# Kernel tuning notes

Measured on AMD Instinct MI355X. Metric: run time of the kernel, lower is better.

## Reference

```python
import jax, jax.numpy as jnp
import numpy as np

N_HEAD, DIM, D_K, D_V = 16, 1024, 64, 64
B, L = 4, 2048


def setup_inputs() -> dict:
    key = jax.random.key(0)
    ks = jax.random.split(key, 8)
    def xavier(k, shape, fan_in, fan_out):
        std = float(np.sqrt(2.0 / (fan_in + fan_out)))
        return jax.random.normal(k, shape, dtype=jnp.float32) * std
    return {
        "q": jax.random.normal(ks[0], (B, L, DIM), dtype=jnp.float32),
        "k": jax.random.normal(ks[1], (B, L, DIM), dtype=jnp.float32),
        "v": jax.random.normal(ks[2], (B, L, DIM), dtype=jnp.float32),
        "w_q": xavier(ks[3], (N_HEAD, DIM, D_K), DIM, D_K),
        "w_k": xavier(ks[4], (N_HEAD, DIM, D_K), DIM, D_K),
        "w_v": xavier(ks[5], (N_HEAD, DIM, D_V), DIM, D_V),
        "proj_w": xavier(ks[6], (DIM, N_HEAD * D_V), N_HEAD * D_V, DIM),
        "proj_b": jnp.zeros((DIM,), dtype=jnp.float32),
    }


def reference(q, k, v, w_q, w_k, w_v, proj_w, proj_b):
    batch, len_q, dim = q.shape
    # NOTE: original scales by sqrt(dim) (model dim), not sqrt(d_k)
    scale = jnp.asarray(np.sqrt(dim), dtype=q.dtype)
    # per-head projections: [h, b, q, dk]
    qh = jnp.einsum('bqd,hdk->hbqk', q, w_q)
    kh = jnp.einsum('bsd,hdk->hbsk', k, w_k)
    vh = jnp.einsum('bsd,hdv->hbsv', v, w_v)
    scores = jnp.einsum('hbqk,hbsk->hbqs', qh, kh) / scale
    attn = jax.nn.softmax(scores, axis=-1)
    out = jnp.einsum('hbqs,hbsv->hbqv', attn, vh)
    # concat heads along last dim: [b, q, h*dv] (head-major order, matching torch.cat(split))
    out = jnp.transpose(out, (1, 2, 0, 3)).reshape(batch, len_q, -1)
    # output projection (dropout is identity at eval)
    return out @ proj_w.T + proj_b
```

## Files before the change

kernel.cpp:

```cpp
#include <hip/hip_runtime.h>
#include <hip/hip_bf16.h>
#include <stdint.h>

#define NH 16
#define DM 1024
#define DKV 64
#define BB 4
#define LL 2048
#define MT (BB*LL)
#define NT (LL/64)

typedef __bf16 bf16;
typedef __bf16 bf16x8 __attribute__((ext_vector_type(8)));
typedef float f32x4 __attribute__((ext_vector_type(4)));
typedef float f32x16 __attribute__((ext_vector_type(16)));
typedef unsigned int u32x2 __attribute__((ext_vector_type(2)));
typedef unsigned int u32x4 __attribute__((ext_vector_type(4)));

__device__ __forceinline__ void gload_lds16(const void* g, void* l) {
  __builtin_amdgcn_global_load_lds(
      (const __attribute__((address_space(1))) unsigned int*)g,
      (__attribute__((address_space(3))) unsigned int*)l, 16, 0, 0);
}

__device__ __forceinline__ unsigned short bfbits(float x) {
  bf16 b = (bf16)x;
  return __builtin_bit_cast(unsigned short, b);
}

__device__ __forceinline__ float fast_exp2(float x) {
#if defined(__has_builtin)
#if __has_builtin(__builtin_amdgcn_exp2f)
  return __builtin_amdgcn_exp2f(x);
#else
  float r; asm("v_exp_f32 %0, %1" : "=v"(r) : "v"(x)); return r;
#endif
#else
  float r; asm("v_exp_f32 %0, %1" : "=v"(r) : "v"(x)); return r;
#endif
}

#if defined(__has_builtin)
#if __has_builtin(__builtin_amdgcn_permlane32_swap)
#define HAVE_PLSWAP 1
#endif
#endif

__device__ __forceinline__ u32x2 plswap(unsigned int a, unsigned int b, int hi) {
#ifdef HAVE_PLSWAP
  auto rr = __builtin_amdgcn_permlane32_swap(a, b, false, false);
  u32x2 r; r.x = rr[0]; r.y = rr[1];
  return r;
#else
  unsigned int pa = (unsigned int)__shfl_xor((int)a, 32);
  unsigned int pb_ = (unsigned int)__shfl_xor((int)b, 32);
  u32x2 r;
  r.x = hi ? pb_ : a;
  r.y = hi ? b : pa;
  return r;
#endif
}

__device__ __forceinline__ bf16x8 pack8(const f32x4& lo, const f32x4& hi2) {
  u32x4 u;
  u.x = (unsigned int)bfbits(lo[0]) | ((unsigned int)bfbits(lo[1]) << 16);
  u.y = (unsigned int)bfbits(lo[2]) | ((unsigned int)bfbits(lo[3]) << 16);
  u.z = (unsigned int)bfbits(hi2[0]) | ((unsigned int)bfbits(hi2[1]) << 16);
  u.w = (unsigned int)bfbits(hi2[2]) | ((unsigned int)bfbits(hi2[3]) << 16);
  return __builtin_bit_cast(bf16x8, u);
}

__global__ __launch_bounds__(256) void prep_w(const float* __restrict__ w0, const float* __restrict__ w1,
                                              const float* __restrict__ w2, const float* __restrict__ pw,
                                              bf16* __restrict__ o0, bf16* __restrict__ o1,
                                              bf16* __restrict__ o2, bf16* __restrict__ Wp) {
  __shared__ float t[64][65];
  if (blockIdx.z < 3) {
    const float* w = blockIdx.z == 0 ? w0 : (blockIdx.z == 1 ? w1 : w2);
    bf16* o = blockIdx.z == 0 ? o0 : (blockIdx.z == 1 ? o1 : o2);
    int h = blockIdx.y, d0 = blockIdx.x * 64;
    const float* src = w + ((size_t)h * DM + d0) * DKV;
    for (int i = threadIdx.x; i < 64 * 64; i += 256) {
      int r = i >> 6, c = i & 63;
      t[r][c] = src[(size_t)r * DKV + c];
    }
    __syncthreads();
    for (int i = threadIdx.x; i < 64 * 64; i += 256) {
      int kk = i >> 6, d = i & 63;
      o[((size_t)(h * 64 + kk)) * DM + d0 + d] = (bf16)t[d][kk];
    }
  } else {
    int base = ((blockIdx.y * 16 + blockIdx.x) * 256 + threadIdx.x) * 2;
#pragma unroll
    for (int e = 0; e < 2; ++e) {
      int i = base + e;
      const float4* p = (const float4*)pw + (size_t)i * 2;
      float4 a = p[0], b = p[1];
      bf16x8 r;
      r[0] = (bf16)a.x; r[1] = (bf16)a.y; r[2] = (bf16)a.z; r[3] = (bf16)a.w;
      r[4] = (bf16)b.x; r[5] = (bf16)b.y; r[6] = (bf16)b.z; r[7] = (bf16)b.w;
      *((bf16x8*)Wp + i) = r;
    }
  }
}

__global__ __launch_bounds__(256, 3) void gemm_qkv(const float* __restrict__ Qf, const float* __restrict__ Kf,
                                                   const float* __restrict__ Vf, const bf16* __restrict__ Wqt,
                                                   const bf16* __restrict__ Wkt, const bf16* __restrict__ Wvt,
                                                   bf16* __restrict__ QH, bf16* __restrict__ KH,
                                                   bf16* __restrict__ VT) {
  __shared__ bf16 sA[128 * 64];
  __shared__ bf16 sB[128 * 64];
  const int bid = blockIdx.x;
  const int xcd = bid & 7;
  const int j   = bid >> 3;
  const int nb  = j & 7;
  const int t   = j >> 3;
  const int mb  = xcd + 8 * (t & 7);
  const int mode = t >> 3;
  const float* A = mode == 0 ? Qf : (mode == 1 ? Kf : Vf);
  const bf16* Bt = mode == 0 ? Wqt : (mode == 1 ? Wkt : Wvt);
  const int tid = threadIdx.x;
  const int w = tid >> 6, l = tid & 63;
  const int c = l & 15, g4 = l >> 4;
  const int wm = w >> 1, wn = w & 1;
  const int m0 = mb * 128, n0 = nb * 128;

  int grow[4], gsg[4];
#pragma unroll
  for (int jj = 0; jj < 4; ++jj) {
    int gi = jj * 256 + tid;
    grow[jj] = gi >> 3;
    gsg[jj] = (gi & 7) ^ (grow[jj] & 7);
  }

  f32x4 ra[4][2];
  u32x4 rbr[4];

  auto LOADA = [&](int kt) {
#pragma unroll
    for (int jj = 0; jj < 4; ++jj) {
      const float* s = A + (size_t)(m0 + grow[jj]) * 1024 + kt + gsg[jj] * 8;
      ra[jj][0] = *(const f32x4*)s;
      ra[jj][1] = *(const f32x4*)(s + 4);
    }
  };
  auto LOADB = [&](int kt) {
#pragma unroll
    for (int jj = 0; jj < 4; ++jj)
      rbr[jj] = *(const u32x4*)(Bt + (size_t)(n0 + grow[jj]) * 1024 + kt + gsg[jj] * 8);
  };
  auto WRITE = [&]() {
#pragma unroll
    for (int jj = 0; jj < 4; ++jj) {
      *(bf16x8*)((char*)sA + (jj * 256 + tid) * 16) = pack8(ra[jj][0], ra[jj][1]);
      *(u32x4*)((char*)sB + (jj * 256 + tid) * 16) = rbr[jj];
    }
  };

  f32x4 acc[4][4] = {};
  LOADA(0); LOADB(0);
  for (int it = 0; it < 16; ++it) {
    WRITE();
    if (it < 15) { LOADA((it + 1) * 64); LOADB((it + 1) * 64); }
    asm volatile("s_waitcnt lgkmcnt(0)" ::: "memory");
    __builtin_amdgcn_s_barrier();
#pragma unroll
    for (int ks = 0; ks < 2; ++ks) {
      bf16x8 af[4], bfr[4];
#pragma unroll
      for (int x = 0; x < 4; ++x) {
        int ar = wm * 64 + x * 16 + c;
        af[x] = *(const bf16x8*)((const char*)sA + ar * 128 + (((ks * 4 + g4) ^ (ar & 7)) * 16));
        int br = wn * 64 + x * 16 + c;
        bfr[x] = *(const bf16x8*)((const char*)sB + br * 128 + (((ks * 4 + g4) ^ (br & 7)) * 16));
      }
      __builtin_amdgcn_s_setprio(1);
#pragma unroll
      for (int x = 0; x < 4; ++x)
#pragma unroll
        for (int y = 0; y < 4; ++y)
          acc[x][y] = __builtin_amdgcn_mfma_f32_16x16x32_bf16(af[x], bfr[y], acc[x][y], 0, 0, 0);
      __builtin_amdgcn_s_setprio(0);
    }
    __builtin_amdgcn_s_barrier();
  }

  const int mm = m0 + wm * 64, nn = n0 + wn * 64;
  if (mode < 2) {
    bf16* O = mode == 0 ? QH : KH;
    const float s = (mode == 0) ? 0.03125f * 1.44269504088896f : 1.0f;
#pragma unroll
    for (int x = 0; x < 4; ++x)
#pragma unroll
      for (int y = 0; y < 4; ++y)
#pragma unroll
        for (int r = 0; r < 4; ++r) {
          int m = mm + x * 16 + g4 * 4 + r;
          int n = nn + y * 16 + c;
          O[(size_t)m * 1024 + n] = (bf16)(acc[x][y][r] * s);
        }
  } else {
    bf16* O = VT;
#pragma unroll
    for (int x = 0; x < 4; ++x)
#pragma unroll
      for (int y = 0; y < 4; ++y) {
        int mb2 = mm + x * 16 + g4 * 4;
        int n = nn + y * 16 + c;
        int bb2 = mb2 >> 11, sidx = mb2 & 2047;
        int hh2 = n >> 6, dv = n & 63;
        unsigned int u0 = bfbits(acc[x][y][0]) | ((unsigned int)bfbits(acc[x][y][1]) << 16);
        unsigned int u1 = bfbits(acc[x][y][2]) | ((unsigned int)bfbits(acc[x][y][3]) << 16);
        *(uint2*)(O + ((size_t)((hh2 * 4 + bb2) * 64 + dv)) * LL + sidx) = make_uint2(u0, u1);
      }
  }
}

__global__ __launch_bounds__(256) void gemm_proj(const bf16* __restrict__ A, const bf16* __restrict__ Bt,
                                                 float* __restrict__ Out, const float* __restrict__ bias) {
  __shared__ bf16 sA[128 * 64];
  __shared__ bf16 sB[128 * 64];
  const int bid = blockIdx.x;
  const int xcd = bid & 7;
  const int j = bid >> 3;
  const int nb = j & 7;
  const int mb = xcd + 8 * (j >> 3);
  const int tid = threadIdx.x;
  const int w = tid >> 6, l = tid & 63;
  const int c = l & 15, g4 = l >> 4;
  const int wm = w >> 1, wn = w & 1;
  const int m0 = mb * 128, n0 = nb * 128;

  f32x4 acc[4][4] = {};
  for (int kt = 0; kt < 1024; kt += 64) {
#pragma unroll
    for (int i = 0; i < 4; ++i) {
      int blk = i * 4 + w;
      int row = blk * 8 + (l >> 3);
      int g = (l & 7) ^ (row & 7);
      gload_lds16(A + ((size_t)(m0 + row)) * 1024 + kt + g * 8, (char*)sA + blk * 1024);
      gload_lds16(Bt + ((size_t)(n0 + row)) * 1024 + kt + g * 8, (char*)sB + blk * 1024);
    }
    __syncthreads();
#pragma unroll
    for (int ks = 0; ks < 2; ++ks) {
      bf16x8 af[4], bfr[4];
#pragma unroll
      for (int x = 0; x < 4; ++x) {
        int ar = wm * 64 + x * 16 + c;
        af[x] = *(const bf16x8*)((const char*)sA + ar * 128 + (((ks * 4 + g4) ^ (ar & 7)) * 16));
        int br = wn * 64 + x * 16 + c;
        bfr[x] = *(const bf16x8*)((const char*)sB + br * 128 + (((ks * 4 + g4) ^ (br & 7)) * 16));
      }
#pragma unroll
      for (int x = 0; x < 4; ++x)
#pragma unroll
        for (int y = 0; y < 4; ++y)
          acc[x][y] = __builtin_amdgcn_mfma_f32_16x16x32_bf16(af[x], bfr[y], acc[x][y], 0, 0, 0);
    }
    __syncthreads();
  }

  const int mm = m0 + wm * 64, nn = n0 + wn * 64;
#pragma unroll
  for (int x = 0; x < 4; ++x)
#pragma unroll
    for (int y = 0; y < 4; ++y)
#pragma unroll
      for (int r = 0; r < 4; ++r) {
        int m = mm + x * 16 + g4 * 4 + r;
        int n = nn + y * 16 + c;
        Out[(size_t)m * 1024 + n] = acc[x][y][r] + bias[n];
      }
}

__global__ __launch_bounds__(256, 2) void attn_kernel(const bf16* __restrict__ qh,
                                                      const bf16* __restrict__ kh,
                                                      const bf16* __restrict__ vt,
                                                      bf16* __restrict__ o) {
  __shared__ bf16 sK[4][64 * 64];
  __shared__ bf16 sV[4][64 * 64];
  const int tid = threadIdx.x, w = tid >> 6, l = tid & 63;
  const int c = l & 31, hi = l >> 5;
  const int bh = blockIdx.x, b = bh & 3, h = bh >> 2;
  const int q0 = blockIdx.y * 256 + w * 64;

  const bf16* qbase = qh + ((size_t)(b * LL)) * DM + h * 64;
  const bf16* kbase = kh + ((size_t)(b * LL)) * DM + h * 64;
  const bf16* vbase = vt + ((size_t)((h * 4 + b) * 64)) * LL;

  bf16x8 qfA[4], qfB[4];
#pragma unroll
  for (int ks = 0; ks < 4; ++ks) {
    qfA[ks] = *(const bf16x8*)(qbase + (size_t)(q0 + c) * DM + ks * 16 + hi * 8);
    qfB[ks] = *(const bf16x8*)(qbase + (size_t)(q0 + 32 + c) * DM + ks * 16 + hi * 8);
  }

  bf16x8 onesf;
#pragma unroll
  for (int i = 0; i < 8; ++i) onesf[i] = (bf16)1.0f;

  f32x16 oA0 = {}, oA1 = {}, oB0 = {}, oB1 = {};
  f32x16 lAa = {}, lBa = {};

  auto STAGE = [&](int bufi, int kv0) {
#pragma unroll
    for (int j = 0; j < 2; ++j) {
      int gi = w * 128 + j * 64 + l;
      int row = gi >> 3;
      int g = (gi & 7) ^ (row & 7);
      gload_lds16(kbase + (size_t)(kv0 + row) * DM + g * 8,
                  (char*)sK[bufi] + (w * 128 + j * 64) * 16);
      gload_lds16(vbase + (size_t)row * LL + kv0 + g * 8,
                  (char*)sV[bufi] + (w * 128 + j * 64) * 16);
    }
  };

  auto EXPPACK = [&](f32x16& st0, f32x16& st1, bf16x8* pb) {
#pragma unroll
    for (int r = 0; r < 16; ++r) st0[r] = fast_exp2(st0[r]);
#pragma unroll
    for (int r = 0; r < 16; ++r) st1[r] = fast_exp2(st1[r]);
#pragma unroll
    for (int t = 0; t < 2; ++t) {
      const f32x16& st = t ? st1 : st0;
      unsigned int u[4][2];
#pragma unroll
      for (int g2 = 0; g2 < 4; ++g2) {
        u[g2][0] = (unsigned int)bfbits(st[4 * g2 + 0]) | ((unsigned int)bfbits(st[4 * g2 + 1]) << 16);
        u[g2][1] = (unsigned int)bfbits(st[4 * g2 + 2]) | ((unsigned int)bfbits(st[4 * g2 + 3]) << 16);
      }
      u32x2 s0 = plswap(u[0][0], u[1][0], hi);
      u32x2 s1 = plswap(u[0][1], u[1][1], hi);
      u32x4 w0; w0.x = s0.x; w0.y = s1.x; w0.z = s0.y; w0.w = s1.y;
      pb[2 * t] = __builtin_bit_cast(bf16x8, w0);
      u32x2 s2 = plswap(u[2][0], u[3][0], hi);
      u32x2 s3 = plswap(u[2][1], u[3][1], hi);
      u32x4 w1; w1.x = s2.x; w1.y = s3.x; w1.z = s2.y; w1.w = s3.y;
      pb[2 * t + 1] = __builtin_bit_cast(bf16x8, w1);
    }
  };

  auto TILE = [&](int bufi) {
    const char* Kb = (const char*)sK[bufi];
    const char* Vb = (const char*)sV[bufi];

    bf16x8 kf[8];
#pragma unroll
    for (int ks = 0; ks < 4; ++ks) {
      int slot = ((ks * 2 + hi) ^ (c & 7)) * 16;
      kf[ks]     = *(const bf16x8*)(Kb + c * 128 + slot);
      kf[4 + ks] = *(const bf16x8*)(Kb + (32 + c) * 128 + slot);
    }
    f32x16 sA0 = {}, sA1 = {}, sB0 = {}, sB1 = {};
    __builtin_amdgcn_s_setprio(1);
#pragma unroll
    for (int ks = 0; ks < 4; ++ks) {
      sA0 = __builtin_amdgcn_mfma_f32_32x32x16_bf16(kf[ks],     qfA[ks], sA0, 0, 0, 0);
      sA1 = __builtin_amdgcn_mfma_f32_32x32x16_bf16(kf[4 + ks], qfA[ks], sA1, 0, 0, 0);
    }
#pragma unroll
    for (int ks = 0; ks < 4; ++ks) {
      sB0 = __builtin_amdgcn_mfma_f32_32x32x16_bf16(kf[ks],     qfB[ks], sB0, 0, 0, 0);
      sB1 = __builtin_amdgcn_mfma_f32_32x32x16_bf16(kf[4 + ks], qfB[ks], sB1, 0, 0, 0);
    }
    __builtin_amdgcn_s_setprio(0);

    bf16x8 pbA[4];
    EXPPACK(sA0, sA1, pbA);

    bf16x8 vf[8];
#pragma unroll
    for (int ks = 0; ks < 4; ++ks) {
      int slot = ((ks * 2 + hi) ^ (c & 7)) * 16;
      vf[ks]     = *(const bf16x8*)(Vb + c * 128 + slot);
      vf[4 + ks] = *(const bf16x8*)(Vb + (32 + c) * 128 + slot);
    }
    __builtin_amdgcn_s_setprio(1);
#pragma unroll
    for (int ks = 0; ks < 4; ++ks) {
      oA0 = __builtin_amdgcn_mfma_f32_32x32x16_bf16(vf[ks],     pbA[ks], oA0, 0, 0, 0);
      oA1 = __builtin_amdgcn_mfma_f32_32x32x16_bf16(vf[4 + ks], pbA[ks], oA1, 0, 0, 0);
      lAa = __builtin_amdgcn_mfma_f32_32x32x16_bf16(onesf,      pbA[ks], lAa, 0, 0, 0);
    }
    __builtin_amdgcn_s_setprio(0);

    bf16x8 pbB[4];
    EXPPACK(sB0, sB1, pbB);
    __builtin_amdgcn_s_setprio(1);
#pragma unroll
    for (int ks = 0; ks < 4; ++ks) {
      oB0 = __builtin_amdgcn_mfma_f32_32x32x16_bf16(vf[ks],     pbB[ks], oB0, 0, 0, 0);
      oB1 = __builtin_amdgcn_mfma_f32_32x32x16_bf16(vf[4 + ks], pbB[ks], oB1, 0, 0, 0);
      lBa = __builtin_amdgcn_mfma_f32_32x32x16_bf16(onesf,      pbB[ks], lBa, 0, 0, 0);
    }
    __builtin_amdgcn_s_setprio(0);
  };

  STAGE(0, 0);
  STAGE(1, 64);

  for (int wd = 0; wd < 16; ++wd) {
    __builtin_amdgcn_s_barrier();
    int t2 = 2 * wd + 2;
    if (t2 < NT) {
      STAGE(t2 & 3, t2 * 64);
      STAGE((t2 + 1) & 3, (t2 + 1) * 64);
      asm volatile("s_waitcnt vmcnt(8)" ::: "memory");
    } else {
      asm volatile("s_waitcnt vmcnt(0)" ::: "memory");
    }
    TILE((2 * wd) & 3);
    TILE((2 * wd + 1) & 3);
  }

  bf16* ob = o + ((size_t)(b * LL)) * DM + h * 64;
  {
    float inv = 1.0f / lAa[0];
#pragma unroll
    for (int dt = 0; dt < 2; ++dt) {
      const f32x16& oc = dt ? oA1 : oA0;
#pragma unroll
      for (int rg = 0; rg < 4; ++rg) {
        int dv0 = dt * 32 + rg * 8 + hi * 4;
        unsigned int u0 = (unsigned int)bfbits(oc[rg * 4 + 0] * inv) |
                          ((unsigned int)bfbits(oc[rg * 4 + 1] * inv) << 16);
        unsigned int u1 = (unsigned int)bfbits(oc[rg * 4 + 2] * inv) |
                          ((unsigned int)bfbits(oc[rg * 4 + 3] * inv) << 16);
        *(uint2*)(ob + (size_t)(q0 + c) * DM + dv0) = make_uint2(u0, u1);
      }
    }
  }
  {
    float inv = 1.0f / lBa[0];
#pragma unroll
    for (int dt = 0; dt < 2; ++dt) {
      const f32x16& oc = dt ? oB1 : oB0;
#pragma unroll
      for (int rg = 0; rg < 4; ++rg) {
        int dv0 = dt * 32 + rg * 8 + hi * 4;
        unsigned int u0 = (unsigned int)bfbits(oc[rg * 4 + 0] * inv) |
                          ((unsigned int)bfbits(oc[rg * 4 + 1] * inv) << 16);
        unsigned int u1 = (unsigned int)bfbits(oc[rg * 4 + 2] * inv) |
                          ((unsigned int)bfbits(oc[rg * 4 + 3] * inv) << 16);
        *(uint2*)(ob + (size_t)(q0 + 32 + c) * DM + dv0) = make_uint2(u0, u1);
      }
    }
  }
}

extern "C" void kernel_launch(void* const* d_in, const int* in_sizes, int n_in,
                              void* d_out, int out_size, void* d_ws, size_t ws_size,
                              hipStream_t stream) {
  const float* q  = (const float*)d_in[0];
  const float* k  = (const float*)d_in[1];
  const float* v  = (const float*)d_in[2];
  const float* wq = (const float*)d_in[3];
  const float* wk = (const float*)d_in[4];
  const float* wv = (const float*)d_in[5];
  const float* pw = (const float*)d_in[6];
  const float* pb = (const float*)d_in[7];
  float* out = (float*)d_out;

  char* ws = (char*)d_ws;
  const size_t SX = (size_t)MT * DM * 2;
  const size_t SW = (size_t)DM * DM * 2;
  bf16* Wqt = (bf16*)(ws);
  bf16* Wkt = (bf16*)(ws + SW);
  bf16* Wvt = (bf16*)(ws + 2 * SW);
  bf16* Wp  = (bf16*)(ws + 3 * SW);
  bf16* QH  = (bf16*)(ws + 4 * SW);
  bf16* KH  = (bf16*)(ws + 4 * SW + SX);
  bf16* VT  = (bf16*)(ws + 4 * SW + 2 * SX);
  bf16* OO  = (bf16*)(ws + 4 * SW + 3 * SX);

  prep_w<<<dim3(16, 16, 4), 256, 0, stream>>>(wq, wk, wv, pw, Wqt, Wkt, Wvt, Wp);

  gemm_qkv<<<dim3(1536), 256, 0, stream>>>(q, k, v, Wqt, Wkt, Wvt, QH, KH, VT);

  attn_kernel<<<dim3(64, 8), 256, 0, stream>>>(QH, KH, VT, OO);

  gemm_proj<<<dim3(512), 256, 0, stream>>>(OO, Wp, out, pb);
}
```

Measured before the change: 189.3 us.

## Double-buffer LDS tiles in QKV projection GEMM to halve barriers

The QKV projection GEMM now uses two LDS buffers per operand and alternates between them. Each iteration writes the next tile while computing on the current one, leaving one barrier per k-step instead of two. LDS use doubles from 32KB to 64KB per block, which may cut occupancy below the launch_bounds target of 3 blocks per CU.

```diff
diff --git a/kernel.cpp b/kernel.cpp
--- a/kernel.cpp
+++ b/kernel.cpp
@@ -109,8 +109,8 @@
                                                    const bf16* __restrict__ Wkt, const bf16* __restrict__ Wvt,
                                                    bf16* __restrict__ QH, bf16* __restrict__ KH,
                                                    bf16* __restrict__ VT) {
-  __shared__ bf16 sA[128 * 64];
-  __shared__ bf16 sB[128 * 64];
+  __shared__ bf16 sA0[128 * 64], sA1[128 * 64];
+  __shared__ bf16 sB0[128 * 64], sB1[128 * 64];
   const int bid = blockIdx.x;
   const int xcd = bid & 7;
   const int j   = bid >> 3;
@@ -150,30 +150,27 @@
     for (int jj = 0; jj < 4; ++jj)
       rbr[jj] = *(const u32x4*)(Bt + (size_t)(n0 + grow[jj]) * 1024 + kt + gsg[jj] * 8);
   };
-  auto WRITE = [&]() {
+  auto WRITEX = [&](bf16* dA, bf16* dB) {
 #pragma unroll
     for (int jj = 0; jj < 4; ++jj) {
-      *(bf16x8*)((char*)sA + (jj * 256 + tid) * 16) = pack8(ra[jj][0], ra[jj][1]);
-      *(u32x4*)((char*)sB + (jj * 256 + tid) * 16) = rbr[jj];
+      *(bf16x8*)((char*)dA + (jj * 256 + tid) * 16) = pack8(ra[jj][0], ra[jj][1]);
+      *(u32x4*)((char*)dB + (jj * 256 + tid) * 16) = rbr[jj];
     }
   };
 
   f32x4 acc[4][4] = {};
-  LOADA(0); LOADB(0);
-  for (int it = 0; it < 16; ++it) {
-    WRITE();
-    if (it < 15) { LOADA((it + 1) * 64); LOADB((it + 1) * 64); }
-    asm volatile("s_waitcnt lgkmcnt(0)" ::: "memory");
-    __builtin_amdgcn_s_barrier();
+  auto COMPUTE = [&](const bf16* Ab_, const bf16* Bb_) {
+    const char* Ab = (const char*)Ab_;
+    const char* Bb = (const char*)Bb_;
 #pragma unroll
     for (int ks = 0; ks < 2; ++ks) {
       bf16x8 af[4], bfr[4];
 #pragma unroll
       for (int x = 0; x < 4; ++x) {
         int ar = wm * 64 + x * 16 + c;
-        af[x] = *(const bf16x8*)((const char*)sA + ar * 128 + (((ks * 4 + g4) ^ (ar & 7)) * 16));
+        af[x] = *(const bf16x8*)(Ab + ar * 128 + (((ks * 4 + g4) ^ (ar & 7)) * 16));
         int br = wn * 64 + x * 16 + c;
-        bfr[x] = *(const bf16x8*)((const char*)sB + br * 128 + (((ks * 4 + g4) ^ (br & 7)) * 16));
+        bfr[x] = *(const bf16x8*)(Bb + br * 128 + (((ks * 4 + g4) ^ (br & 7)) * 16));
       }
       __builtin_amdgcn_s_setprio(1);
 #pragma unroll
@@ -183,7 +180,27 @@
           acc[x][y] = __builtin_amdgcn_mfma_f32_16x16x32_bf16(af[x], bfr[y], acc[x][y], 0, 0, 0);
       __builtin_amdgcn_s_setprio(0);
     }
+  };
+
+  LOADA(0); LOADB(0);
+  WRITEX(sA0, sB0);
+  LOADA(64); LOADB(64);
+  asm volatile("s_waitcnt lgkmcnt(0)" ::: "memory");
+  __builtin_amdgcn_s_barrier();
+
+  for (int it = 0; it < 16; it += 2) {
+    if (it + 1 < 16) WRITEX(sA1, sB1);
+    if (it + 2 < 16) { LOADA((it + 2) * 64); LOADB((it + 2) * 64); }
+    COMPUTE(sA0, sB0);
+    asm volatile("s_waitcnt lgkmcnt(0)" ::: "memory");
     __builtin_amdgcn_s_barrier();
+    if (it + 1 < 16) {
+      if (it + 2 < 16) WRITEX(sA0, sB0);
+      if (it + 3 < 16) { LOADA((it + 3) * 64); LOADB((it + 3) * 64); }
+      COMPUTE(sA1, sB1);
+      asm volatile("s_waitcnt lgkmcnt(0)" ::: "memory");
+      __builtin_amdgcn_s_barrier();
+    }
   }
 
   const int mm = m0 + wm * 64, nn = n0 + wn * 64;
```

Result: slower. 198.3 us (+4.8%).
